# Performance work log

Measured on AMD Instinct MI355X. Metric: run time of the kernel, lower is better.

The kernel has to match this reference:

```python
import jax, jax.numpy as jnp
import numpy as np

N_VARS, T, N_GRID, C = 8, 4, 12288, 16
B, V, NH = 1, 4, 9
UP, E = 16, 64  # 4**(zoom-emb_zoom)=16, embed_dim=64


def setup_inputs() -> dict:
    key = jax.random.key(0)
    k1, k2, k3, k4 = jax.random.split(key, 4)
    mg_emb = jax.random.normal(k1, (N_VARS, T, N_GRID, C), dtype=jnp.float32)
    var_indices = jax.random.randint(k2, (B, V), 0, N_VARS)
    adjc = jax.random.randint(k3, (N_GRID, NH), 0, N_GRID)
    # get_layer([nh, C], [UP, E]): dense mapping nh*C -> UP*E (scaled init)
    W = jax.random.normal(k4, (NH * C, UP * E), dtype=jnp.float32) / np.sqrt(NH * C)
    b = jnp.zeros((UP * E,), dtype=jnp.float32)
    return {"mg_emb": mg_emb, "var_indices": var_indices, "adjc": adjc, "W": W, "b": b}


def reference(mg_emb, var_indices, adjc, W, b):
    # variable-index embedding lookup: [B,V,T,N_GRID,C]
    embs = mg_emb[var_indices]
    # irregular neighbor gather over grid adjacency: [B,V,T,P,NH,C]
    nb = embs[:, :, :, adjc, :]
    Bv, Vv, Tv, P = nb.shape[:4]
    x = nb.reshape(Bv, Vv, Tv, P, NH * C)  # flatten neighborhood patch
    # patch MLP: [nh*C] -> [UP*E]
    y = jnp.einsum('bvtpf,fo->bvtpo', x, W) + b
    # final view: [B,V,T,P*UP,E]
    return y.reshape(Bv, Vv, Tv, P * UP, E)
```

## Files before the change

### kernel.cpp

```cpp
#include <hip/hip_runtime.h>
#include <hip/hip_bf16.h>
#include <stdint.h>

#define T_DIM   4
#define N_GRID  12288
#define C_DIM   16
#define NH      9
#define N_OUT   1024
#define K_DIM   144
#define M_TOTAL 196608
#define MG_ELEMS (8 * T_DIM * N_GRID * C_DIM)

#define AS_STRIDE 146
#define KSTEPS    9

typedef __attribute__((ext_vector_type(4)))  float    f32x4;
typedef __attribute__((ext_vector_type(16))) float    f32x16;
typedef __attribute__((ext_vector_type(4)))  _Float16 f16x4;
typedef __attribute__((ext_vector_type(8)))  _Float16 f16x8;

__global__ void pack_w_kernel(const float* __restrict__ W,
                              _Float16* __restrict__ Wpk) {
    const int gid  = blockIdx.x * blockDim.x + threadIdx.x;
    const int cg   = gid & 1;
    const int lane = (gid >> 1) & 63;
    const int q    = (gid >> 7) & 15;
    const int s    = gid >> 11;
    const int l31  = lane & 31;
    const int lhi  = lane >> 5;

    _Float16 v[8];
#pragma unroll
    for (int j = 0; j < 8; ++j) {
        const int k   = 16 * s + 8 * lhi + j;
        const int col = q * 64 + cg * 32 + l31;
        v[j] = (_Float16)W[k * N_OUT + col];
    }
    *(f16x8*)(Wpk + (size_t)gid * 8) = *(const f16x8*)v;
}

__global__ void conv_mg_kernel(const float* __restrict__ mg,
                               _Float16* __restrict__ mgh) {
    const size_t n4 = MG_ELEMS / 4;
    const size_t stride = (size_t)gridDim.x * blockDim.x;
    for (size_t i = (size_t)blockIdx.x * blockDim.x + threadIdx.x; i < n4; i += stride) {
        f32x4 f = *(const f32x4*)(mg + 4 * i);
        f16x4 h;
#pragma unroll
        for (int j = 0; j < 4; ++j) h[j] = (_Float16)f[j];
        *(f16x4*)(mgh + 4 * i) = h;
    }
}

__global__ __launch_bounds__(512, 4) void mg_gemm_kernel(
    const _Float16* __restrict__ mgh,
    const int*   __restrict__ vidx,
    const int*   __restrict__ adjc,
    const _Float16* __restrict__ Wpk,
    const float* __restrict__ bias,
    float* __restrict__ out)
{
    __shared__ _Float16 As[64 * AS_STRIDE];

    const int b     = blockIdx.x;
    const int xcd   = b & 7;
    const int j     = b >> 3;
    const int sl    = j / 384;
    const int jj    = j - sl * 384;
    const int slice = xcd * 2 + sl;
    const int mloc  = jj >> 1;
    const int ytile = jj & 1;

    const int v     = slice >> 2;
    const int t     = slice & 3;
    const int p0    = mloc * 64;
    const int r0    = slice * N_GRID + p0;
    const int vi    = vidx[v];
    const _Float16* src = mgh + (size_t)(vi * T_DIM + t) * N_GRID * C_DIM;

    const int tid = threadIdx.x;

    for (int task = tid; task < 64 * NH; task += 512) {
        const int row = task / NH;
        const int nh  = task - row * NH;
        const int g   = adjc[p0 * NH + task];
        const _Float16* sp = src + (size_t)g * C_DIM;
        _Float16* dst = As + row * AS_STRIDE + nh * C_DIM;
        *(f16x8*)dst       = *(const f16x8*)sp;
        *(f16x8*)(dst + 8) = *(const f16x8*)(sp + 8);
    }
    __syncthreads();

    const int lane = tid & 63;
    const int w    = tid >> 6;
    const int l31  = lane & 31;
    const int lhi  = lane >> 5;
    const int q    = ytile * 8 + w;

    f32x16 acc00, acc01, acc10, acc11;
#pragma unroll
    for (int i = 0; i < 16; ++i) { acc00[i]=0.f; acc01[i]=0.f; acc10[i]=0.f; acc11[i]=0.f; }

    const _Float16* arow0 = As + l31 * AS_STRIDE + 8 * lhi;
    const _Float16* arow1 = arow0 + 32 * AS_STRIDE;
    const _Float16* wp    = Wpk + ((size_t)q * 64 + lane) * 16;

#pragma unroll
    for (int s = 0; s < KSTEPS; ++s) {
        f16x8 a0 = *(const f16x8*)(arow0 + s * C_DIM);
        f16x8 a1 = *(const f16x8*)(arow1 + s * C_DIM);
        const _Float16* bp = wp + (size_t)s * (16 * 64 * 16);
        f16x8 b0 = *(const f16x8*)(bp + 0);
        f16x8 b1 = *(const f16x8*)(bp + 8);
        acc00 = __builtin_amdgcn_mfma_f32_32x32x16_f16(a0, b0, acc00, 0, 0, 0);
        acc01 = __builtin_amdgcn_mfma_f32_32x32x16_f16(a1, b0, acc01, 0, 0, 0);
        acc10 = __builtin_amdgcn_mfma_f32_32x32x16_f16(a0, b1, acc10, 0, 0, 0);
        acc11 = __builtin_amdgcn_mfma_f32_32x32x16_f16(a1, b1, acc11, 0, 0, 0);
    }

    const int colbase = q * 64 + l31;
    const float b0f = bias[colbase];
    const float b1f = bias[colbase + 32];
    float* outp = out + (size_t)r0 * N_OUT;

#pragma unroll
    for (int r = 0; r < 16; ++r) {
        const int rr = (r & 3) + 8 * (r >> 2) + 4 * lhi;
        __builtin_nontemporal_store(acc00[r] + b0f, &outp[(size_t)rr * N_OUT + colbase]);
        __builtin_nontemporal_store(acc10[r] + b1f, &outp[(size_t)rr * N_OUT + colbase + 32]);
        __builtin_nontemporal_store(acc01[r] + b0f, &outp[(size_t)(rr + 32) * N_OUT + colbase]);
        __builtin_nontemporal_store(acc11[r] + b1f, &outp[(size_t)(rr + 32) * N_OUT + colbase + 32]);
    }
}

extern "C" void kernel_launch(void* const* d_in, const int* in_sizes, int n_in,
                              void* d_out, int out_size, void* d_ws, size_t ws_size,
                              hipStream_t stream) {
    const float* mg   = (const float*)d_in[0];
    const int*   vidx = (const int*)  d_in[1];
    const int*   adjc = (const int*)  d_in[2];
    const float* W    = (const float*)d_in[3];
    const float* bias = (const float*)d_in[4];
    float*       out  = (float*)d_out;

    _Float16* Wpk = (_Float16*)d_ws;
    _Float16* mgh = (_Float16*)((char*)d_ws + (1 << 20));

    pack_w_kernel<<<dim3(72), dim3(256), 0, stream>>>(W, Wpk);
    conv_mg_kernel<<<dim3(1024), dim3(256), 0, stream>>>(mg, mgh);

    mg_gemm_kernel<<<dim3(M_TOTAL / 64 * 2), dim3(512), 0, stream>>>(
        mgh, vidx, adjc, Wpk, bias, out);
}
```

Before: 151.8 us.

## Fuse fp32-to-fp16 conversion into gather and split MFMA accumulation into row halves

Drops the separate kernel that converted the whole mg_emb tensor to fp16. The gather now reads fp32 neighbour rows directly and converts them into shared memory, which removes a launch and a full pass over the tensor. The GEMM loop is also restructured to compute and store two 32-row halves one after another, so only two accumulators are live instead of four. This lowers register pressure but reloads the B operands for each half and doubles the gather read bytes per row.

```diff
diff --git a/kernel.cpp b/kernel.cpp
--- a/kernel.cpp
+++ b/kernel.cpp
@@ -9,7 +9,6 @@
 #define N_OUT   1024
 #define K_DIM   144
 #define M_TOTAL 196608
-#define MG_ELEMS (8 * T_DIM * N_GRID * C_DIM)
 
 #define AS_STRIDE 146
 #define KSTEPS    9
@@ -39,21 +38,8 @@
     *(f16x8*)(Wpk + (size_t)gid * 8) = *(const f16x8*)v;
 }
 
-__global__ void conv_mg_kernel(const float* __restrict__ mg,
-                               _Float16* __restrict__ mgh) {
-    const size_t n4 = MG_ELEMS / 4;
-    const size_t stride = (size_t)gridDim.x * blockDim.x;
-    for (size_t i = (size_t)blockIdx.x * blockDim.x + threadIdx.x; i < n4; i += stride) {
-        f32x4 f = *(const f32x4*)(mg + 4 * i);
-        f16x4 h;
-#pragma unroll
-        for (int j = 0; j < 4; ++j) h[j] = (_Float16)f[j];
-        *(f16x4*)(mgh + 4 * i) = h;
-    }
-}
-
 __global__ __launch_bounds__(512, 4) void mg_gemm_kernel(
-    const _Float16* __restrict__ mgh,
+    const float* __restrict__ mg,
     const int*   __restrict__ vidx,
     const int*   __restrict__ adjc,
     const _Float16* __restrict__ Wpk,
@@ -76,7 +62,7 @@
     const int p0    = mloc * 64;
     const int r0    = slice * N_GRID + p0;
     const int vi    = vidx[v];
-    const _Float16* src = mgh + (size_t)(vi * T_DIM + t) * N_GRID * C_DIM;
+    const float* src = mg + (size_t)(vi * T_DIM + t) * N_GRID * C_DIM;
 
     const int tid = threadIdx.x;
 
@@ -84,10 +70,22 @@
         const int row = task / NH;
         const int nh  = task - row * NH;
         const int g   = adjc[p0 * NH + task];
-        const _Float16* sp = src + (size_t)g * C_DIM;
+        const float* sp = src + (size_t)g * C_DIM;
+        f32x4 f0 = *(const f32x4*)(sp + 0);
+        f32x4 f1 = *(const f32x4*)(sp + 4);
+        f32x4 f2 = *(const f32x4*)(sp + 8);
+        f32x4 f3 = *(const f32x4*)(sp + 12);
+        f16x8 h0, h1;
+#pragma unroll
+        for (int i = 0; i < 4; ++i) {
+            h0[i]     = (_Float16)f0[i];
+            h0[i + 4] = (_Float16)f1[i];
+            h1[i]     = (_Float16)f2[i];
+            h1[i + 4] = (_Float16)f3[i];
+        }
         _Float16* dst = As + row * AS_STRIDE + nh * C_DIM;
-        *(f16x8*)dst       = *(const f16x8*)sp;
-        *(f16x8*)(dst + 8) = *(const f16x8*)(sp + 8);
+        *(f16x8*)dst       = h0;
+        *(f16x8*)(dst + 8) = h1;
     }
     __syncthreads();
 
@@ -97,39 +95,35 @@
     const int lhi  = lane >> 5;
     const int q    = ytile * 8 + w;
 
-    f32x16 acc00, acc01, acc10, acc11;
-#pragma unroll
-    for (int i = 0; i < 16; ++i) { acc00[i]=0.f; acc01[i]=0.f; acc10[i]=0.f; acc11[i]=0.f; }
-
-    const _Float16* arow0 = As + l31 * AS_STRIDE + 8 * lhi;
-    const _Float16* arow1 = arow0 + 32 * AS_STRIDE;
-    const _Float16* wp    = Wpk + ((size_t)q * 64 + lane) * 16;
+    const _Float16* wp = Wpk + ((size_t)q * 64 + lane) * 16;
+    const int colbase  = q * 64 + l31;
+    const float b0f = bias[colbase];
+    const float b1f = bias[colbase + 32];
 
 #pragma unroll
-    for (int s = 0; s < KSTEPS; ++s) {
-        f16x8 a0 = *(const f16x8*)(arow0 + s * C_DIM);
-        f16x8 a1 = *(const f16x8*)(arow1 + s * C_DIM);
-        const _Float16* bp = wp + (size_t)s * (16 * 64 * 16);
-        f16x8 b0 = *(const f16x8*)(bp + 0);
-        f16x8 b1 = *(const f16x8*)(bp + 8);
-        acc00 = __builtin_amdgcn_mfma_f32_32x32x16_f16(a0, b0, acc00, 0, 0, 0);
-        acc01 = __builtin_amdgcn_mfma_f32_32x32x16_f16(a1, b0, acc01, 0, 0, 0);
-        acc10 = __builtin_amdgcn_mfma_f32_32x32x16_f16(a0, b1, acc10, 0, 0, 0);
-        acc11 = __builtin_amdgcn_mfma_f32_32x32x16_f16(a1, b1, acc11, 0, 0, 0);
-    }
+    for (int h = 0; h < 2; ++h) {
+        f32x16 accA, accB;
+#pragma unroll
+        for (int i = 0; i < 16; ++i) { accA[i] = 0.f; accB[i] = 0.f; }
 
-    const int colbase = q * 64 + l31;
-    const float b0f = bias[colbase];
-    const float b1f = bias[colbase + 32];
-    float* outp = out + (size_t)r0 * N_OUT;
+        const _Float16* arow = As + (32 * h + l31) * AS_STRIDE + 8 * lhi;
+#pragma unroll
+        for (int s = 0; s < KSTEPS; ++s) {
+            f16x8 a = *(const f16x8*)(arow + s * C_DIM);
+            const _Float16* bp = wp + (size_t)s * (16 * 64 * 16);
+            f16x8 b0 = *(const f16x8*)(bp + 0);
+            f16x8 b1 = *(const f16x8*)(bp + 8);
+            accA = __builtin_amdgcn_mfma_f32_32x32x16_f16(a, b0, accA, 0, 0, 0);
+            accB = __builtin_amdgcn_mfma_f32_32x32x16_f16(a, b1, accB, 0, 0, 0);
+        }
 
+        float* outp = out + (size_t)(r0 + 32 * h) * N_OUT;
 #pragma unroll
-    for (int r = 0; r < 16; ++r) {
-        const int rr = (r & 3) + 8 * (r >> 2) + 4 * lhi;
-        __builtin_nontemporal_store(acc00[r] + b0f, &outp[(size_t)rr * N_OUT + colbase]);
-        __builtin_nontemporal_store(acc10[r] + b1f, &outp[(size_t)rr * N_OUT + colbase + 32]);
-        __builtin_nontemporal_store(acc01[r] + b0f, &outp[(size_t)(rr + 32) * N_OUT + colbase]);
-        __builtin_nontemporal_store(acc11[r] + b1f, &outp[(size_t)(rr + 32) * N_OUT + colbase + 32]);
+        for (int r = 0; r < 16; ++r) {
+            const int rr = (r & 3) + 8 * (r >> 2) + 4 * lhi;
+            __builtin_nontemporal_store(accA[r] + b0f, &outp[(size_t)rr * N_OUT + colbase]);
+            __builtin_nontemporal_store(accB[r] + b1f, &outp[(size_t)rr * N_OUT + colbase + 32]);
+        }
     }
 }
 
@@ -144,11 +138,9 @@
     float*       out  = (float*)d_out;
 
     _Float16* Wpk = (_Float16*)d_ws;
-    _Float16* mgh = (_Float16*)((char*)d_ws + (1 << 20));
 
     pack_w_kernel<<<dim3(72), dim3(256), 0, stream>>>(W, Wpk);
-    conv_mg_kernel<<<dim3(1024), dim3(256), 0, stream>>>(mg, mgh);
 
     mg_gemm_kernel<<<dim3(M_TOTAL / 64 * 2), dim3(512), 0, stream>>>(
-        mgh, vidx, adjc, Wpk, bias, out);
+        mg, vidx, adjc, Wpk, bias, out);
 }
```

Result: slower. 161.7 us (+6.5%).
